# Performance work log

Hardware: AMD Instinct MI355X
Metric: run time of the kernel (lower is better)

The kernel has to match this reference:

```python
import jax, jax.numpy as jnp
import numpy as np

N = 50000       # nodes
E = 800000      # edges (avg degree 16)
IN_FEATS = 256
HEADS = 8
OUT_FEATS = 32
SLOPE = 0.2     # LeakyReLU negative slope


def setup_inputs() -> dict:
    key = jax.random.key(0)
    k1, k2, k3, k4, k5, k6 = jax.random.split(key, 6)
    feat = jax.random.normal(k1, (N, IN_FEATS), dtype=jnp.float32)
    # xavier-ish scaling for the linear weight, stored [in, out] for jax
    fc_w = jax.random.normal(k2, (IN_FEATS, HEADS * OUT_FEATS), dtype=jnp.float32) / np.sqrt(IN_FEATS)
    attn_l = jax.random.normal(k3, (HEADS, OUT_FEATS), dtype=jnp.float32) * 0.1
    attn_r = jax.random.normal(k4, (HEADS, OUT_FEATS), dtype=jnp.float32) * 0.1
    src = jax.random.randint(k5, (E,), 0, N, dtype=jnp.int32)
    dst = jnp.sort(jax.random.randint(k6, (E,), 0, N, dtype=jnp.int32))
    return {"feat": feat, "fc_w": fc_w, "attn_l": attn_l, "attn_r": attn_r,
            "src": src, "dst": dst}


def reference(feat, fc_w, attn_l, attn_r, src, dst):
    # dense projection: [N, H, F]
    feat_src = (feat @ fc_w).reshape(N, HEADS, OUT_FEATS)
    el = jnp.einsum('nhf,hf->nh', feat_src, attn_l)   # [N, H]
    er = jnp.einsum('nhf,hf->nh', feat_src, attn_r)   # [N, H]

    # per-edge raw score: nb.el + v.er  -> [E, H]
    e = el[src] + er[dst]
    # per-destination max over incoming edges (edge softmax stabilizer)
    m = jax.ops.segment_max(e, dst, num_segments=N)   # [N, H]
    z = e - m[dst]
    # Seastar order: exp(leaky_relu(emb - max(embs)))
    coeff = jnp.exp(jnp.where(z >= 0, z, SLOPE * z))  # [E, H]
    s = jax.ops.segment_sum(coeff, dst, num_segments=N)
    alpha = coeff / s[dst]                            # [E, H]

    # weighted scatter-sum of gathered neighbor features -> [N, H, F]
    out = jax.ops.segment_sum(alpha[:, :, None] * feat_src[src], dst, num_segments=N)
    return out
```

## Files before the change

kernel.cpp:

```cpp
#include <hip/hip_runtime.h>
#include <hip/hip_bf16.h>

#define N_NODES 50000
#define N_EDGES 800000
#define IN_F 256
#define HEADS 8
#define OUT_F 32
#define HF (HEADS * OUT_F)
#define SLOPE 0.2f

typedef __attribute__((ext_vector_type(8))) short bf16x8;
typedef __attribute__((ext_vector_type(4))) float f32x4;

__device__ __forceinline__ ushort f2bf(float f) {
  union { float f; unsigned u; } x;
  x.f = f;
  unsigned r = x.u + 0x7FFFu + ((x.u >> 16) & 1u);
  return (ushort)(r >> 16);
}

__device__ __forceinline__ float bf2f_lo(unsigned u) {
  return __uint_as_float(u << 16);
}
__device__ __forceinline__ float bf2f_hi(unsigned u) {
  return __uint_as_float(u & 0xFFFF0000u);
}

#define ROWPTR_BLOCKS ((N_NODES + 1 + 255) / 256)

__global__ __launch_bounds__(256) void prep_kernel(
    const float* __restrict__ fc_w, const float* __restrict__ attn_l,
    ushort* __restrict__ Bt, float* __restrict__ wl,
    const int* __restrict__ dst, int* __restrict__ row_ptr) {
  __shared__ float tile[32][33];
  const int b = blockIdx.x;
  const int t = threadIdx.x;

  if (b < 64) {
    const int bx = (b & 7) * 32;
    const int by = (b >> 3) * 32;
    const int tx = t & 31;
    const int ty = t >> 5;
#pragma unroll
    for (int i = 0; i < 32; i += 8)
      tile[ty + i][tx] = fc_w[(size_t)(by + ty + i) * HF + bx + tx];
    __syncthreads();
#pragma unroll
    for (int i = 0; i < 32; i += 8)
      Bt[(size_t)(bx + ty + i) * IN_F + by + tx] = f2bf(tile[tx][ty + i]);
  } else if (b == 64) {
#pragma unroll
    for (int ii = 0; ii < 8; ++ii) {
      const int idx = ii * 256 + t;
      const int k = idx >> 3;
      const int h = idx & 7;
      const float* fp = &fc_w[(size_t)k * HF + h * OUT_F];
      const float* ap = &attn_l[h * OUT_F];
      float acc = 0.f;
#pragma unroll
      for (int f = 0; f < OUT_F; f += 4) {
        float4 a = *(const float4*)&fp[f];
        float4 bb = *(const float4*)&ap[f];
        acc += a.x * bb.x + a.y * bb.y + a.z * bb.z + a.w * bb.w;
      }
      wl[idx] = acc;
    }
  } else {
    const int i = (b - 65) * 256 + t;
    if (i <= N_NODES) {
      int lo = 0, hi = N_EDGES;
      while (lo < hi) {
        int mid = (lo + hi) >> 1;
        if (dst[mid] < i) lo = mid + 1; else hi = mid;
      }
      row_ptr[i] = lo;
    }
  }
}

#define BM 64
#define BN 256
#define BK 32
#define LDA 40

__global__ __launch_bounds__(256) void gemm_mfma(
    const float* __restrict__ A, const ushort* __restrict__ Bt,
    ushort* __restrict__ Cb, int M) {
  __shared__ __align__(16) ushort As[BM * LDA];
  __shared__ __align__(16) ushort Bs[BN * LDA];

  const int t = threadIdx.x;
  const int wave = t >> 6;
  const int lane = t & 63;
  const int m0 = blockIdx.x * BM;

  const int ar = t >> 2;
  const int ak = (t & 3) * 8;
  const int br = t >> 2;
  const int bk = (t & 3) * 8;

  const int q = lane >> 4;
  const int l16 = lane & 15;
  const int wn = wave * 64;

  f32x4 acc[4][4] = {};

  for (int k0 = 0; k0 < IN_F; k0 += BK) {
    {
      float4 v0 = make_float4(0.f, 0.f, 0.f, 0.f);
      float4 v1 = make_float4(0.f, 0.f, 0.f, 0.f);
      if (m0 + ar < M) {
        const float* ap = &A[(size_t)(m0 + ar) * IN_F + k0 + ak];
        v0 = *(const float4*)ap;
        v1 = *(const float4*)(ap + 4);
      }
      union { ushort s[8]; uint4 v; } u;
      u.s[0] = f2bf(v0.x); u.s[1] = f2bf(v0.y);
      u.s[2] = f2bf(v0.z); u.s[3] = f2bf(v0.w);
      u.s[4] = f2bf(v1.x); u.s[5] = f2bf(v1.y);
      u.s[6] = f2bf(v1.z); u.s[7] = f2bf(v1.w);
      *(uint4*)&As[ar * LDA + ak] = u.v;
    }
#pragma unroll
    for (int i = 0; i < 4; ++i) {
      const int n = br + i * 64;
      *(uint4*)&Bs[n * LDA + bk] =
          *(const uint4*)&Bt[(size_t)n * IN_F + k0 + bk];
    }
    __syncthreads();

    bf16x8 aF[4], bF[4];
#pragma unroll
    for (int i = 0; i < 4; ++i)
      aF[i] = *(const bf16x8*)&As[(i * 16 + l16) * LDA + q * 8];
#pragma unroll
    for (int jj = 0; jj < 4; ++jj)
      bF[jj] = *(const bf16x8*)&Bs[(wn + jj * 16 + l16) * LDA + q * 8];
#pragma unroll
    for (int i = 0; i < 4; ++i)
#pragma unroll
      for (int jj = 0; jj < 4; ++jj)
        acc[i][jj] = __builtin_amdgcn_mfma_f32_16x16x32_bf16(
            aF[i], bF[jj], acc[i][jj], 0, 0, 0);
    __syncthreads();
  }

#pragma unroll
  for (int i = 0; i < 4; ++i) {
#pragma unroll
    for (int r = 0; r < 4; ++r) {
      const int row = m0 + 16 * i + q * 4 + r;
      if (row < M) {
#pragma unroll
        for (int jj = 0; jj < 4; ++jj) {
          const int col = wn + 16 * jj + l16;
          Cb[(size_t)row * HF + col] = f2bf(acc[i][jj][r]);
        }
      }
    }
  }
}

__global__ __launch_bounds__(256) void el_kernel(
    const float* __restrict__ feat, const float* __restrict__ wl,
    float* __restrict__ el, int NH) {
  __shared__ __align__(16) float wlsT[HEADS][IN_F + 4];
  const int t = threadIdx.x;
#pragma unroll
  for (int i = 0; i < (IN_F * HEADS) / 256; ++i) {
    const int idx = i * 256 + t;
    wlsT[idx & 7][idx >> 3] = wl[idx];
  }
  __syncthreads();

  const int idx = blockIdx.x * 256 + t;
  if (idx >= NH) return;
  const int n = idx >> 3;
  const int h = idx & 7;
  const float* fp = &feat[(size_t)n * IN_F];
  const float* wp = &wlsT[h][0];
  float acc = 0.f;
#pragma unroll 8
  for (int k0 = 0; k0 < IN_F; k0 += 4) {
    float4 v = *(const float4*)&fp[k0];
    float4 w = *(const float4*)&wp[k0];
    acc += v.x * w.x + v.y * w.y + v.z * w.z + v.w * w.w;
  }
  el[idx] = acc;
}

__global__ __launch_bounds__(256) void aggregate_kernel(
    const ushort* __restrict__ featb, const float* __restrict__ el,
    const int* __restrict__ src, const int* __restrict__ row_ptr,
    float* __restrict__ out) {
  const int v = blockIdx.x;
  const int t = threadIdx.x;
  const int beg = row_ptr[v];
  const int deg = row_ptr[v + 1] - beg;

  if (deg == 0) {
    out[(size_t)v * HF + t] = 0.f;
    return;
  }

  __shared__ float s_wred[8][HEADS];
  __shared__ __align__(16) float s_alpha[64][HEADS];
  __shared__ int s_src[64];
  __shared__ __align__(16) float s_out[4][HF];

  const int lane = t & 63;
  const int wave = t >> 6;
  const int j = t >> 3;
  const int h8 = t & 7;
  const int h = lane >> 3;

  float4 acc = make_float4(0.f, 0.f, 0.f, 0.f);
  float ssum = 0.f;

  if (deg <= 64) {
    const int nIter = (deg > wave) ? ((deg - wave + 3) >> 2) : 0;
    uint2 q[16];
#pragma unroll
    for (int i = 0; i < 16; ++i) {
      if (i < nIter) {
        const int s = src[beg + wave + 4 * i];
        q[i] = *(const uint2*)&featb[(size_t)s * HF + lane * 4];
      }
    }
    float v1 = 0.f, v2 = 0.f;
    float mx = -1e30f;
    if (j < deg) {
      v1 = el[(size_t)src[beg + j] * HEADS + h8];
      mx = v1;
    }
    if (j + 32 < deg) {
      v2 = el[(size_t)src[beg + j + 32] * HEADS + h8];
      mx = fmaxf(mx, v2);
    }
    mx = fmaxf(mx, __shfl_xor(mx, 8));
    mx = fmaxf(mx, __shfl_xor(mx, 16));
    mx = fmaxf(mx, __shfl_xor(mx, 32));
    if (lane < HEADS) s_wred[wave][lane] = mx;
    __syncthreads();
    const float m = fmaxf(fmaxf(s_wred[0][h8], s_wred[1][h8]),
                          fmaxf(s_wred[2][h8], s_wred[3][h8]));
    if (j < deg) {
      const float z = v1 - m;
      const float w = (z >= 0.f) ? z : SLOPE * z;
      const float cf = __expf(w);
      s_alpha[j][h8] = cf;
      ssum += cf;
    }
    if (j + 32 < deg) {
      const float z = v2 - m;
      const float w = (z >= 0.f) ? z : SLOPE * z;
      const float cf = __expf(w);
      s_alpha[j + 32][h8] = cf;
      ssum += cf;
    }
    __syncthreads();
#pragma unroll
    for (int i = 0; i < 16; ++i) {
      if (i < nIter) {
        const float a = s_alpha[wave + 4 * i][h];
        acc.x = fmaf(a, bf2f_lo(q[i].x), acc.x);
        acc.y = fmaf(a, bf2f_hi(q[i].x), acc.y);
        acc.z = fmaf(a, bf2f_lo(q[i].y), acc.z);
        acc.w = fmaf(a, bf2f_hi(q[i].y), acc.w);
      }
    }
  } else {
    float mx = -1e30f;
    for (int e = j; e < deg; e += 32)
      mx = fmaxf(mx, el[(size_t)src[beg + e] * HEADS + h8]);
    mx = fmaxf(mx, __shfl_xor(mx, 8));
    mx = fmaxf(mx, __shfl_xor(mx, 16));
    mx = fmaxf(mx, __shfl_xor(mx, 32));
    if (lane < HEADS) s_wred[wave][lane] = mx;
    __syncthreads();
    const float m = fmaxf(fmaxf(s_wred[0][h8], s_wred[1][h8]),
                          fmaxf(s_wred[2][h8], s_wred[3][h8]));

    for (int c0 = 0; c0 < deg; c0 += 64) {
      const int cn = min(64, deg - c0);
      const int cnp = (cn + 3) & ~3;
      __syncthreads();
      for (int cc = j; cc < cnp; cc += 32) {
        if (cc < cn) {
          const int s = src[beg + c0 + cc];
          if (h8 == 0) s_src[cc] = s;
          const float z = el[(size_t)s * HEADS + h8] - m;
          const float w = (z >= 0.f) ? z : SLOPE * z;
          const float cf = __expf(w);
          s_alpha[cc][h8] = cf;
          ssum += cf;
        } else {
          if (h8 == 0) s_src[cc] = 0;
          s_alpha[cc][h8] = 0.f;
        }
      }
      __syncthreads();
#pragma unroll 2
      for (int e0 = 0; e0 < cnp; e0 += 4) {
        const int e = e0 + wave;
        const int s = s_src[e];
        const float a = s_alpha[e][h];
        const uint2 u = *(const uint2*)&featb[(size_t)s * HF + lane * 4];
        acc.x = fmaf(a, bf2f_lo(u.x), acc.x);
        acc.y = fmaf(a, bf2f_hi(u.x), acc.y);
        acc.z = fmaf(a, bf2f_lo(u.y), acc.z);
        acc.w = fmaf(a, bf2f_hi(u.y), acc.w);
      }
    }
  }

  ssum += __shfl_xor(ssum, 8);
  ssum += __shfl_xor(ssum, 16);
  ssum += __shfl_xor(ssum, 32);
  if (lane < HEADS) s_wred[4 + wave][lane] = ssum;
  *(float4*)&s_out[wave][lane * 4] = acc;
  __syncthreads();

  const int ho = t >> 5;
  const float ssum_all =
      s_wred[4][ho] + s_wred[5][ho] + s_wred[6][ho] + s_wred[7][ho];
  const float r = s_out[0][t] + s_out[1][t] + s_out[2][t] + s_out[3][t];
  out[(size_t)v * HF + t] = r / ssum_all;
}

extern "C" void kernel_launch(void* const* d_in, const int* in_sizes, int n_in,
                              void* d_out, int out_size, void* d_ws,
                              size_t ws_size, hipStream_t stream) {
  const float* feat = (const float*)d_in[0];
  const float* fc_w = (const float*)d_in[1];
  const float* attn_l = (const float*)d_in[2];
  const int* src = (const int*)d_in[4];
  const int* dst = (const int*)d_in[5];
  float* out = (float*)d_out;

  const int N = N_NODES;

  ushort* featb = (ushort*)d_ws;
  float* el = (float*)(featb + (size_t)N * HF);
  float* wl = el + (size_t)N * HEADS;
  ushort* Bt = (ushort*)(wl + IN_F * HEADS);
  int* row_ptr = (int*)(Bt + (size_t)IN_F * HF);

  prep_kernel<<<65 + ROWPTR_BLOCKS, 256, 0, stream>>>(fc_w, attn_l, Bt, wl,
                                                      dst, row_ptr);

  gemm_mfma<<<(N + BM - 1) / BM, 256, 0, stream>>>(feat, Bt, featb, N);

  el_kernel<<<(N * HEADS + 255) / 256, 256, 0, stream>>>(feat, wl, el,
                                                         N * HEADS);

  aggregate_kernel<<<N, 256, 0, stream>>>(featb, el, src, row_ptr, out);
}
```

Baseline: 264.3 us.

## Map one wavefront per destination node in aggregation, replacing shared memory with shuffles

The aggregation kernel now assigns each 64-lane wave its own destination node, four nodes per block, instead of one 256-thread block per node. The per-head max, the softmax coefficients and the neighbor indices are passed between lanes with shuffles rather than through shared memory and block barriers, and the final per-head normalization is done in-wave. The aim is to remove the __syncthreads calls, the shared-memory traffic and the cross-wave reduction. The cost is that each wave now walks all of a node's edges serially, so fewer gathers are in flight per node and waves may be imbalanced across degrees. Separately, the el kernel keeps its weights in shared memory in their original layout and indexes them directly instead of transposing them.

```diff
diff --git a/kernel.cpp b/kernel.cpp
--- a/kernel.cpp
+++ b/kernel.cpp
@@ -164,13 +164,11 @@
 __global__ __launch_bounds__(256) void el_kernel(
     const float* __restrict__ feat, const float* __restrict__ wl,
     float* __restrict__ el, int NH) {
-  __shared__ __align__(16) float wlsT[HEADS][IN_F + 4];
+  __shared__ float wls[IN_F * HEADS];
   const int t = threadIdx.x;
 #pragma unroll
-  for (int i = 0; i < (IN_F * HEADS) / 256; ++i) {
-    const int idx = i * 256 + t;
-    wlsT[idx & 7][idx >> 3] = wl[idx];
-  }
+  for (int i = 0; i < (IN_F * HEADS) / 256; ++i)
+    wls[i * 256 + t] = wl[i * 256 + t];
   __syncthreads();
 
   const int idx = blockIdx.x * 256 + t;
@@ -178,13 +176,12 @@
   const int n = idx >> 3;
   const int h = idx & 7;
   const float* fp = &feat[(size_t)n * IN_F];
-  const float* wp = &wlsT[h][0];
   float acc = 0.f;
 #pragma unroll 8
   for (int k0 = 0; k0 < IN_F; k0 += 4) {
     float4 v = *(const float4*)&fp[k0];
-    float4 w = *(const float4*)&wp[k0];
-    acc += v.x * w.x + v.y * w.y + v.z * w.z + v.w * w.w;
+    acc += v.x * wls[(k0 + 0) * 8 + h] + v.y * wls[(k0 + 1) * 8 + h] +
+           v.z * wls[(k0 + 2) * 8 + h] + v.w * wls[(k0 + 3) * 8 + h];
   }
   el[idx] = acc;
 }
@@ -193,119 +190,98 @@
     const ushort* __restrict__ featb, const float* __restrict__ el,
     const int* __restrict__ src, const int* __restrict__ row_ptr,
     float* __restrict__ out) {
-  const int v = blockIdx.x;
   const int t = threadIdx.x;
+  const int wave = t >> 6;
+  const int lane = t & 63;
+  const int v = blockIdx.x * 4 + wave;
+
   const int beg = row_ptr[v];
   const int deg = row_ptr[v + 1] - beg;
 
+  const int j = lane >> 3;
+  const int h8 = lane & 7;
+
+  float4 acc = make_float4(0.f, 0.f, 0.f, 0.f);
+
   if (deg == 0) {
-    out[(size_t)v * HF + t] = 0.f;
+    *(float4*)&out[(size_t)v * HF + lane * 4] = acc;
     return;
   }
 
-  __shared__ float s_wred[8][HEADS];
-  __shared__ __align__(16) float s_alpha[64][HEADS];
-  __shared__ int s_src[64];
-  __shared__ __align__(16) float s_out[4][HF];
-
-  const int lane = t & 63;
-  const int wave = t >> 6;
-  const int j = t >> 3;
-  const int h8 = t & 7;
-  const int h = lane >> 3;
-
-  float4 acc = make_float4(0.f, 0.f, 0.f, 0.f);
   float ssum = 0.f;
 
   if (deg <= 64) {
-    const int nIter = (deg > wave) ? ((deg - wave + 3) >> 2) : 0;
-    uint2 q[16];
-#pragma unroll
-    for (int i = 0; i < 16; ++i) {
-      if (i < nIter) {
-        const int s = src[beg + wave + 4 * i];
-        q[i] = *(const uint2*)&featb[(size_t)s * HF + lane * 4];
-      }
-    }
-    float v1 = 0.f, v2 = 0.f;
+    const int npass = (deg + 7) >> 3;
+    int sidx[8];
+    float vel[8];
     float mx = -1e30f;
-    if (j < deg) {
-      v1 = el[(size_t)src[beg + j] * HEADS + h8];
-      mx = v1;
-    }
-    if (j + 32 < deg) {
-      v2 = el[(size_t)src[beg + j + 32] * HEADS + h8];
-      mx = fmaxf(mx, v2);
+#pragma unroll
+    for (int p = 0; p < 8; ++p) {
+      if (p < npass) {
+        const int e = p * 8 + j;
+        if (e < deg) {
+          sidx[p] = src[beg + e];
+          vel[p] = el[(size_t)sidx[p] * HEADS + h8];
+        } else {
+          sidx[p] = 0;
+          vel[p] = -1e30f;
+        }
+        mx = fmaxf(mx, vel[p]);
+      }
     }
     mx = fmaxf(mx, __shfl_xor(mx, 8));
     mx = fmaxf(mx, __shfl_xor(mx, 16));
     mx = fmaxf(mx, __shfl_xor(mx, 32));
-    if (lane < HEADS) s_wred[wave][lane] = mx;
-    __syncthreads();
-    const float m = fmaxf(fmaxf(s_wred[0][h8], s_wred[1][h8]),
-                          fmaxf(s_wred[2][h8], s_wred[3][h8]));
-    if (j < deg) {
-      const float z = v1 - m;
-      const float w = (z >= 0.f) ? z : SLOPE * z;
-      const float cf = __expf(w);
-      s_alpha[j][h8] = cf;
-      ssum += cf;
-    }
-    if (j + 32 < deg) {
-      const float z = v2 - m;
-      const float w = (z >= 0.f) ? z : SLOPE * z;
-      const float cf = __expf(w);
-      s_alpha[j + 32][h8] = cf;
-      ssum += cf;
-    }
-    __syncthreads();
-#pragma unroll
-    for (int i = 0; i < 16; ++i) {
-      if (i < nIter) {
-        const float a = s_alpha[wave + 4 * i][h];
-        acc.x = fmaf(a, bf2f_lo(q[i].x), acc.x);
-        acc.y = fmaf(a, bf2f_hi(q[i].x), acc.y);
-        acc.z = fmaf(a, bf2f_lo(q[i].y), acc.z);
-        acc.w = fmaf(a, bf2f_hi(q[i].y), acc.w);
+
+#pragma unroll
+    for (int p = 0; p < 8; ++p) {
+      if (p < npass) {
+        float cf = 0.f;
+        if (p * 8 + j < deg) {
+          const float z = vel[p] - mx;
+          const float w = (z >= 0.f) ? z : SLOPE * z;
+          cf = __expf(w);
+        }
+        ssum += cf;
+        const int emax = min(8, deg - p * 8);
+#pragma unroll
+        for (int ee = 0; ee < 8; ++ee) {
+          if (ee < emax) {
+            const float a = __shfl(cf, ee * 8 + j);
+            const int sb = __shfl(sidx[p], ee * 8);
+            const uint2 u =
+                *(const uint2*)&featb[(size_t)sb * HF + lane * 4];
+            acc.x = fmaf(a, bf2f_lo(u.x), acc.x);
+            acc.y = fmaf(a, bf2f_hi(u.x), acc.y);
+            acc.z = fmaf(a, bf2f_lo(u.y), acc.z);
+            acc.w = fmaf(a, bf2f_hi(u.y), acc.w);
+          }
+        }
       }
     }
   } else {
     float mx = -1e30f;
-    for (int e = j; e < deg; e += 32)
+    for (int e = j; e < deg; e += 8)
       mx = fmaxf(mx, el[(size_t)src[beg + e] * HEADS + h8]);
     mx = fmaxf(mx, __shfl_xor(mx, 8));
     mx = fmaxf(mx, __shfl_xor(mx, 16));
     mx = fmaxf(mx, __shfl_xor(mx, 32));
-    if (lane < HEADS) s_wred[wave][lane] = mx;
-    __syncthreads();
-    const float m = fmaxf(fmaxf(s_wred[0][h8], s_wred[1][h8]),
-                          fmaxf(s_wred[2][h8], s_wred[3][h8]));
-
-    for (int c0 = 0; c0 < deg; c0 += 64) {
-      const int cn = min(64, deg - c0);
-      const int cnp = (cn + 3) & ~3;
-      __syncthreads();
-      for (int cc = j; cc < cnp; cc += 32) {
-        if (cc < cn) {
-          const int s = src[beg + c0 + cc];
-          if (h8 == 0) s_src[cc] = s;
-          const float z = el[(size_t)s * HEADS + h8] - m;
-          const float w = (z >= 0.f) ? z : SLOPE * z;
-          const float cf = __expf(w);
-          s_alpha[cc][h8] = cf;
-          ssum += cf;
-        } else {
-          if (h8 == 0) s_src[cc] = 0;
-          s_alpha[cc][h8] = 0.f;
-        }
-      }
-      __syncthreads();
-#pragma unroll 2
-      for (int e0 = 0; e0 < cnp; e0 += 4) {
-        const int e = e0 + wave;
-        const int s = s_src[e];
-        const float a = s_alpha[e][h];
-        const uint2 u = *(const uint2*)&featb[(size_t)s * HF + lane * 4];
+
+    for (int p0 = 0; p0 < deg; p0 += 8) {
+      float cf = 0.f;
+      int sidx = 0;
+      if (p0 + j < deg) {
+        sidx = src[beg + p0 + j];
+        const float z = el[(size_t)sidx * HEADS + h8] - mx;
+        const float w = (z >= 0.f) ? z : SLOPE * z;
+        cf = __expf(w);
+      }
+      ssum += cf;
+      const int emax = min(8, deg - p0);
+      for (int ee = 0; ee < emax; ++ee) {
+        const float a = __shfl(cf, ee * 8 + j);
+        const int sb = __shfl(sidx, ee * 8);
+        const uint2 u = *(const uint2*)&featb[(size_t)sb * HF + lane * 4];
         acc.x = fmaf(a, bf2f_lo(u.x), acc.x);
         acc.y = fmaf(a, bf2f_hi(u.x), acc.y);
         acc.z = fmaf(a, bf2f_lo(u.y), acc.z);
@@ -317,15 +293,9 @@
   ssum += __shfl_xor(ssum, 8);
   ssum += __shfl_xor(ssum, 16);
   ssum += __shfl_xor(ssum, 32);
-  if (lane < HEADS) s_wred[4 + wave][lane] = ssum;
-  *(float4*)&s_out[wave][lane * 4] = acc;
-  __syncthreads();
-
-  const int ho = t >> 5;
-  const float ssum_all =
-      s_wred[4][ho] + s_wred[5][ho] + s_wred[6][ho] + s_wred[7][ho];
-  const float r = s_out[0][t] + s_out[1][t] + s_out[2][t] + s_out[3][t];
-  out[(size_t)v * HF + t] = r / ssum_all;
+  const float inv = 1.0f / __shfl(ssum, j);
+  acc.x *= inv; acc.y *= inv; acc.z *= inv; acc.w *= inv;
+  *(float4*)&out[(size_t)v * HF + lane * 4] = acc;
 }
 
 extern "C" void kernel_launch(void* const* d_in, const int* in_sizes, int n_in,
@@ -354,5 +324,5 @@
   el_kernel<<<(N * HEADS + 255) / 256, 256, 0, stream>>>(feat, wl, el,
                                                          N * HEADS);
 
-  aggregate_kernel<<<N, 256, 0, stream>>>(featb, el, src, row_ptr, out);
-}
+  aggregate_kernel<<<N / 4, 256, 0, stream>>>(featb, el, src, row_ptr, out);
+}
```

Measured after the change: 235.0 us. 11.1% less time.
